# Optimization experiments

Measured on AMD Instinct MI355X. Metric: run time of the kernel, lower is better.

Reference implementation:

```python
import jax, jax.numpy as jnp
import numpy as np

OUT_FEATURES = 4096
IN_FEATURES = 4096
BLOCK_DIM = 16
K = 64
N_BLOCKS = OUT_FEATURES * IN_FEATURES // BLOCK_DIM  # 1,048,576


def setup_inputs() -> dict:
    key = jax.random.key(0)
    k1, k2, k3, k4, k5, k6 = jax.random.split(key, 6)
    x = jax.random.normal(k1, (8192, IN_FEATURES), dtype=jnp.float32)
    coarse_centroids = jax.random.normal(k2, (K, BLOCK_DIM), dtype=jnp.float32)
    coarse_labels = jax.random.randint(k3, (N_BLOCKS,), 0, K, dtype=jnp.int64)
    res_centroids = jax.random.normal(k4, (K, BLOCK_DIM), dtype=jnp.float32) * 0.1
    res_labels = jax.random.randint(k5, (N_BLOCKS,), 0, K, dtype=jnp.int64)
    bias = jax.random.normal(k6, (OUT_FEATURES,), dtype=jnp.float32)
    return {
        'x': x,
        'coarse_centroids': coarse_centroids,
        'coarse_labels': coarse_labels,
        'res_centroids': res_centroids,
        'res_labels': res_labels,
        'bias': bias,
    }


def _dequantize(coarse_centroids, coarse_labels, res_centroids, res_labels):
    # two-level VQ: coarse lookup + residual correction, per block of BLOCK_DIM
    blocks = coarse_centroids[coarse_labels] + res_centroids[res_labels]  # [N_BLOCKS, BLOCK_DIM]
    return blocks.reshape(OUT_FEATURES, IN_FEATURES)


def reference(x, coarse_centroids, coarse_labels, res_centroids, res_labels, bias):
    W = _dequantize(coarse_centroids, coarse_labels, res_centroids, res_labels)
    # F.linear: x @ W.T + bias
    return jnp.dot(x, W.T) + bias
```

## Files before the change

### kernel.cpp

```cpp
#include <hip/hip_runtime.h>
#include <hip/hip_bf16.h>
#include <stdint.h>

#define M_DIM 8192
#define N_DIM 4096
#define K_DIM 4096
#define BM 256
#define BN 256
#define BK2 64
#define NT2 (K_DIM / BK2)
#define THREADS 512
#define NBLOCKS_VQ (N_DIM * K_DIM / 16)

#define TILE_B 32768
#define BBASE  65536
#define SMEM_BYTES 131072

typedef short bf16x8 __attribute__((ext_vector_type(8)));
typedef float f32x4 __attribute__((ext_vector_type(4)));
typedef unsigned short ushort_t;
typedef ushort_t ushort8 __attribute__((ext_vector_type(8)));

#define GLOBAL_AS __attribute__((address_space(1)))
#define LDS_AS __attribute__((address_space(3)))

__device__ __forceinline__ ushort_t f2bf(float f) {
  union { float f; uint32_t u; } v; v.f = f;
  uint32_t u = v.u;
  return (ushort_t)((u + 0x7FFFu + ((u >> 16) & 1u)) >> 16);
}

__global__ __launch_bounds__(256) void dequant_w(
    const float* __restrict__ cc, const int* __restrict__ cl,
    const float* __restrict__ rc, const int* __restrict__ rl,
    ushort_t* __restrict__ wout) {
  int b = blockIdx.x * 256 + threadIdx.x;
  int ci = cl[b];
  int ri = rl[b];
  const float4* c4 = (const float4*)(cc + (size_t)ci * 16);
  const float4* r4 = (const float4*)(rc + (size_t)ri * 16);
  float s[16];
#pragma unroll
  for (int p = 0; p < 4; ++p) {
    float4 a = c4[p];
    float4 r = r4[p];
    s[p * 4 + 0] = a.x + r.x;
    s[p * 4 + 1] = a.y + r.y;
    s[p * 4 + 2] = a.z + r.z;
    s[p * 4 + 3] = a.w + r.w;
  }
  ushort8 o0, o1;
#pragma unroll
  for (int j = 0; j < 8; ++j) o0[j] = f2bf(s[j]);
#pragma unroll
  for (int j = 0; j < 8; ++j) o1[j] = f2bf(s[8 + j]);
  ushort8* dst = (ushort8*)(wout + (size_t)b * 16);
  dst[0] = o0;
  dst[1] = o1;
}

__global__ __launch_bounds__(256) void cvt_x_bf16(const float* __restrict__ x,
                                                  ushort_t* __restrict__ xb) {
  size_t i = (size_t)blockIdx.x * 256 + threadIdx.x;
  const float4* p = (const float4*)x + i * 2;
  float4 a = p[0];
  float4 b = p[1];
  ushort8 o;
  o[0] = f2bf(a.x); o[1] = f2bf(a.y); o[2] = f2bf(a.z); o[3] = f2bf(a.w);
  o[4] = f2bf(b.x); o[5] = f2bf(b.y); o[6] = f2bf(b.z); o[7] = f2bf(b.w);
  ((ushort8*)xb)[i] = o;
}

__device__ __forceinline__ void stage_tile(char* smem,
    const ushort_t* gA0, const ushort_t* gB0, int wbase, int tile, int buf) {
  const ushort_t* ga = gA0 + (size_t)tile * BK2;
  const ushort_t* gb = gB0 + (size_t)tile * BK2;
  char* la = smem + buf * TILE_B + wbase;
  char* lb = smem + BBASE + buf * TILE_B + wbase;
#pragma unroll
  for (int r = 0; r < 4; ++r) {
    __builtin_amdgcn_global_load_lds(
        (const GLOBAL_AS void*)(ga + (size_t)(r * 64) * K_DIM),
        (LDS_AS void*)(la + r * 8192), 16, 0, 0);
    __builtin_amdgcn_global_load_lds(
        (const GLOBAL_AS void*)(gb + (size_t)(r * 64) * K_DIM),
        (LDS_AS void*)(lb + r * 8192), 16, 0, 0);
  }
}

template<int VM, bool ISSUE>
__device__ __forceinline__ void kstep(char* smem,
    const ushort_t* gA0, const ushort_t* gB0, int wbase,
    int aBase, int bBase, f32x4 (&acc)[8][4], int t, int buf) {
  if constexpr (VM == 8) asm volatile("s_waitcnt vmcnt(8)" ::: "memory");
  else asm volatile("s_waitcnt vmcnt(0)" ::: "memory");
  __builtin_amdgcn_s_barrier();
  __builtin_amdgcn_sched_barrier(0);

  const ushort_t* aB = (const ushort_t*)(smem + buf * TILE_B) + aBase;
  const ushort_t* bB = (const ushort_t*)(smem + BBASE + buf * TILE_B) + bBase;

#pragma unroll
  for (int kk = 0; kk < 2; ++kk) {
    bf16x8 b[4], a[8];
#pragma unroll
    for (int n = 0; n < 4; ++n) b[n] = *(const bf16x8*)(bB + kk * 32 + n * 1024);
#pragma unroll
    for (int m = 0; m < 8; ++m) a[m] = *(const bf16x8*)(aB + kk * 32 + m * 1024);
    __builtin_amdgcn_s_setprio(1);
#pragma unroll
    for (int m = 0; m < 8; ++m)
#pragma unroll
      for (int n = 0; n < 4; ++n)
        acc[m][n] = __builtin_amdgcn_mfma_f32_16x16x32_bf16(a[m], b[n], acc[m][n], 0, 0, 0);
    __builtin_amdgcn_s_setprio(0);
  }
  __builtin_amdgcn_s_barrier();
  __builtin_amdgcn_sched_barrier(0);
  if constexpr (ISSUE)
    stage_tile(smem, gA0, gB0, wbase, t + 2, buf);
}

__global__ __launch_bounds__(THREADS, 2) void gemm_bf16(
    const ushort_t* __restrict__ A, const ushort_t* __restrict__ B,
    const float* __restrict__ bias, float* __restrict__ C) {
  extern __shared__ char smem[];

  const int nwg = (M_DIM / BM) * (N_DIM / BN);
  int bid = blockIdx.x;
  int swz = (bid & 7) * (nwg >> 3) + (bid >> 3);
  int bx = swz & 15;
  int by = swz >> 4;
  const int tileM = by * BM;
  const int tileN = bx * BN;

  const int tid = threadIdx.x;
  const int lane = tid & 63;
  const int wave = tid >> 6;
  const int wr = wave >> 2;
  const int wc = wave & 3;

  int srow = tid >> 3;
  int slot = tid & 7;
  int scol = ((slot ^ ((((unsigned)srow >> 2) & 1) << 1)) << 3);
  const ushort_t* gA0 = A + (size_t)(tileM + srow) * K_DIM + scol;
  const ushort_t* gB0 = B + (size_t)(tileN + srow) * K_DIM + scol;
  const int wbase = wave << 10;

  const int lrow = lane & 15;
  const int g8 = (lane >> 4) << 3;
  const int kx = g8 ^ ((lrow & 4) << 2);
  const int aBase = (wr * 128 + lrow) * 64 + kx;
  const int bBase = (wc * 64 + lrow) * 64 + kx;

  f32x4 acc[8][4];
#pragma unroll
  for (int m = 0; m < 8; ++m)
#pragma unroll
    for (int n = 0; n < 4; ++n) acc[m][n] = (f32x4)0.0f;

  stage_tile(smem, gA0, gB0, wbase, 0, 0);
  stage_tile(smem, gA0, gB0, wbase, 1, 1);

  for (int tb = 0; tb < 31; ++tb) {
    kstep<8, true>(smem, gA0, gB0, wbase, aBase, bBase, acc, 2 * tb, 0);
    kstep<8, true>(smem, gA0, gB0, wbase, aBase, bBase, acc, 2 * tb + 1, 1);
  }
  kstep<8, false>(smem, gA0, gB0, wbase, aBase, bBase, acc, 62, 0);
  kstep<0, false>(smem, gA0, gB0, wbase, aBase, bBase, acc, 63, 1);

  const int orow = tileM + wr * 128 + ((lane >> 4) << 2);
  const int ocol0 = tileN + wc * 64 + lrow;
  float bv[4];
#pragma unroll
  for (int n = 0; n < 4; ++n) bv[n] = bias[ocol0 + n * 16];
#pragma unroll
  for (int m = 0; m < 8; ++m) {
#pragma unroll
    for (int n = 0; n < 4; ++n) {
      size_t base = (size_t)(orow + m * 16) * N_DIM + (ocol0 + n * 16);
#pragma unroll
      for (int r = 0; r < 4; ++r)
        C[base + (size_t)r * N_DIM] = acc[m][n][r] + bv[n];
    }
  }
}

extern "C" void kernel_launch(void* const* d_in, const int* in_sizes, int n_in,
                              void* d_out, int out_size, void* d_ws, size_t ws_size,
                              hipStream_t stream) {
  const float* x = (const float*)d_in[0];
  const float* cc = (const float*)d_in[1];
  const int* cl = (const int*)d_in[2];
  const float* rc = (const float*)d_in[3];
  const int* rl = (const int*)d_in[4];
  const float* bias = (const float*)d_in[5];
  float* out = (float*)d_out;

  ushort_t* Wbf = (ushort_t*)d_ws;
  ushort_t* Xbf = (ushort_t*)d_ws + (size_t)N_DIM * K_DIM;

  (void)hipFuncSetAttribute((const void*)gemm_bf16,
                            hipFuncAttributeMaxDynamicSharedMemorySize, SMEM_BYTES);

  dequant_w<<<NBLOCKS_VQ / 256, 256, 0, stream>>>(cc, cl, rc, rl, Wbf);
  cvt_x_bf16<<<(int)((M_DIM * (size_t)K_DIM / 8) / 256), 256, 0, stream>>>(x, Xbf);
  gemm_bf16<<<(M_DIM / BM) * (N_DIM / BN), THREADS, SMEM_BYTES, stream>>>(Xbf, Wbf, bias, out);
}
```

Baseline: 299.4 us.

## Split GEMM k-tile into four quadrant phases interleaving loads with MFMAs

Replaces the two-stage k-step loop, which issued whole-tile prefetches after the compute, with a four-phase k-tile. Each phase reads part of the A/B fragments from LDS, issues part of the next tile's global-to-LDS loads, and runs a quarter of the MFMAs. The LDS swizzle also changes to a full XOR-by-row scheme, and the B rows are remapped so each phase reads one half of the tile. The aim is finer overlap of memory traffic with MFMA work and fewer LDS bank conflicts, at the cost of more barriers per k-tile and a single prefetch tile of lookahead instead of two.

```diff
diff --git a/kernel.cpp b/kernel.cpp
--- a/kernel.cpp
+++ b/kernel.cpp
@@ -7,13 +7,13 @@
 #define K_DIM 4096
 #define BM 256
 #define BN 256
-#define BK2 64
-#define NT2 (K_DIM / BK2)
+#define BK 64
+#define NT (K_DIM / BK)
 #define THREADS 512
 #define NBLOCKS_VQ (N_DIM * K_DIM / 16)
 
-#define TILE_B 32768
-#define BBASE  65536
+#define ABUF_B 32768
+#define BREG   65536
 #define SMEM_BYTES 131072
 
 typedef short bf16x8 __attribute__((ext_vector_type(8)));
@@ -71,54 +71,91 @@
   ((ushort8*)xb)[i] = o;
 }
 
-__device__ __forceinline__ void stage_tile(char* smem,
-    const ushort_t* gA0, const ushort_t* gB0, int wbase, int tile, int buf) {
-  const ushort_t* ga = gA0 + (size_t)tile * BK2;
-  const ushort_t* gb = gB0 + (size_t)tile * BK2;
-  char* la = smem + buf * TILE_B + wbase;
-  char* lb = smem + BBASE + buf * TILE_B + wbase;
-#pragma unroll
-  for (int r = 0; r < 4; ++r) {
-    __builtin_amdgcn_global_load_lds(
-        (const GLOBAL_AS void*)(ga + (size_t)(r * 64) * K_DIM),
-        (LDS_AS void*)(la + r * 8192), 16, 0, 0);
-    __builtin_amdgcn_global_load_lds(
-        (const GLOBAL_AS void*)(gb + (size_t)(r * 64) * K_DIM),
-        (LDS_AS void*)(lb + r * 8192), 16, 0, 0);
-  }
-}
-
-template<int VM, bool ISSUE>
-__device__ __forceinline__ void kstep(char* smem,
-    const ushort_t* gA0, const ushort_t* gB0, int wbase,
-    int aBase, int bBase, f32x4 (&acc)[8][4], int t, int buf) {
-  if constexpr (VM == 8) asm volatile("s_waitcnt vmcnt(8)" ::: "memory");
-  else asm volatile("s_waitcnt vmcnt(0)" ::: "memory");
-  __builtin_amdgcn_s_barrier();
-  __builtin_amdgcn_sched_barrier(0);
-
-  const ushort_t* aB = (const ushort_t*)(smem + buf * TILE_B) + aBase;
-  const ushort_t* bB = (const ushort_t*)(smem + BBASE + buf * TILE_B) + bBase;
-
-#pragma unroll
-  for (int kk = 0; kk < 2; ++kk) {
-    bf16x8 b[4], a[8];
-#pragma unroll
-    for (int n = 0; n < 4; ++n) b[n] = *(const bf16x8*)(bB + kk * 32 + n * 1024);
-#pragma unroll
-    for (int m = 0; m < 8; ++m) a[m] = *(const bf16x8*)(aB + kk * 32 + m * 1024);
-    __builtin_amdgcn_s_setprio(1);
-#pragma unroll
-    for (int m = 0; m < 8; ++m)
-#pragma unroll
-      for (int n = 0; n < 4; ++n)
-        acc[m][n] = __builtin_amdgcn_mfma_f32_16x16x32_bf16(a[m], b[n], acc[m][n], 0, 0, 0);
-    __builtin_amdgcn_s_setprio(0);
-  }
-  __builtin_amdgcn_s_barrier();
-  __builtin_amdgcn_sched_barrier(0);
-  if constexpr (ISSUE)
-    stage_tile(smem, gA0, gB0, wbase, t + 2, buf);
+struct SP {
+  const ushort_t* gA;
+  const ushort_t* gB;
+  char* sm;
+  int wuni;
+};
+
+__device__ __forceinline__ void stA(const SP& s, int r, int tile, int dbuf) {
+  __builtin_amdgcn_global_load_lds(
+      (const GLOBAL_AS void*)(s.gA + (size_t)tile * BK + (size_t)r * 64 * K_DIM),
+      (LDS_AS void*)(s.sm + dbuf * ABUF_B + r * 8192 + s.wuni), 16, 0, 0);
+}
+__device__ __forceinline__ void stB(const SP& s, int r, int tile, int dbuf) {
+  constexpr int roff[4] = {0, 128, 32, 160};
+  __builtin_amdgcn_global_load_lds(
+      (const GLOBAL_AS void*)(s.gB + (size_t)tile * BK + (size_t)roff[r] * K_DIM),
+      (LDS_AS void*)(s.sm + BREG + dbuf * ABUF_B + r * 8192 + s.wuni), 16, 0, 0);
+}
+
+#define BAR()  __builtin_amdgcn_s_barrier()
+#define SCB()  __builtin_amdgcn_sched_barrier(0)
+#define LGKM0() do { asm volatile("s_waitcnt lgkmcnt(0)" ::: "memory"); SCB(); } while (0)
+#define VMC(n) asm volatile("s_waitcnt vmcnt(" #n ")" ::: "memory")
+
+#define MFMA_Q(ACCM, AARR, BARR, ACCN)                                         \
+  __builtin_amdgcn_s_setprio(1);                                               \
+  _Pragma("unroll")                                                            \
+  for (int m = 0; m < 4; ++m)                                                  \
+    _Pragma("unroll")                                                          \
+    for (int ni = 0; ni < 2; ++ni) {                                           \
+      acc[ACCM + m][ACCN + ni] = __builtin_amdgcn_mfma_f32_16x16x32_bf16(      \
+          AARR[m * 2 + 0], BARR[ni * 2 + 0], acc[ACCM + m][ACCN + ni], 0, 0, 0); \
+      acc[ACCM + m][ACCN + ni] = __builtin_amdgcn_mfma_f32_16x16x32_bf16(      \
+          AARR[m * 2 + 1], BARR[ni * 2 + 1], acc[ACCM + m][ACCN + ni], 0, 0, 0); \
+    }                                                                          \
+  __builtin_amdgcn_s_setprio(0);
+
+template<bool ISSUE, int VMP2, int VMP4>
+__device__ __forceinline__ void ktile(const SP& sp, int buf, int t,
+    int aBase, int bBase, int sw0, int sw1, f32x4 (&acc)[8][4]) {
+  const ushort_t* bufA = (const ushort_t*)(sp.sm + buf * ABUF_B);
+  const ushort_t* bufB = (const ushort_t*)(sp.sm + BREG + buf * ABUF_B);
+  bf16x8 a[8], b0[4], b1[4];
+
+#pragma unroll
+  for (int m = 0; m < 4; ++m) {
+    a[m * 2 + 0] = *(const bf16x8*)(bufA + aBase + m * 1024 + sw0);
+    a[m * 2 + 1] = *(const bf16x8*)(bufA + aBase + m * 1024 + sw1);
+  }
+#pragma unroll
+  for (int ni = 0; ni < 2; ++ni) {
+    b0[ni * 2 + 0] = *(const bf16x8*)(bufB + bBase + ni * 1024 + sw0);
+    b0[ni * 2 + 1] = *(const bf16x8*)(bufB + bBase + ni * 1024 + sw1);
+  }
+  if constexpr (ISSUE) { stB(sp, 0, t + 1, buf ^ 1); stB(sp, 1, t + 1, buf ^ 1); }
+  BAR(); LGKM0();
+  MFMA_Q(0, a, b0, 0);
+  BAR(); SCB();
+
+#pragma unroll
+  for (int ni = 0; ni < 2; ++ni) {
+    b1[ni * 2 + 0] = *(const bf16x8*)(bufB + bBase + 8192 + ni * 1024 + sw0);
+    b1[ni * 2 + 1] = *(const bf16x8*)(bufB + bBase + 8192 + ni * 1024 + sw1);
+  }
+  if constexpr (ISSUE) { stB(sp, 2, t + 1, buf ^ 1); stB(sp, 3, t + 1, buf ^ 1); }
+  if constexpr (VMP2 == 4) VMC(4); else VMC(0);
+  BAR(); LGKM0();
+  MFMA_Q(0, a, b1, 2);
+  BAR(); SCB();
+
+#pragma unroll
+  for (int m = 0; m < 4; ++m) {
+    a[m * 2 + 0] = *(const bf16x8*)(bufA + aBase + 4096 + m * 1024 + sw0);
+    a[m * 2 + 1] = *(const bf16x8*)(bufA + aBase + 4096 + m * 1024 + sw1);
+  }
+  if constexpr (ISSUE) { stA(sp, 0, t + 1, buf ^ 1); stA(sp, 2, t + 1, buf ^ 1); }
+  BAR(); LGKM0();
+  MFMA_Q(4, a, b0, 0);
+  BAR(); SCB();
+
+  if constexpr (ISSUE) { stA(sp, 1, t + 1, buf ^ 1); stA(sp, 3, t + 1, buf ^ 1); }
+  if constexpr (VMP4 == 2) VMC(2); else VMC(0);
+  BAR(); LGKM0();
+  MFMA_Q(4, a, b1, 2);
+  BAR(); SCB();
 }
 
 __global__ __launch_bounds__(THREADS, 2) void gemm_bf16(
@@ -137,21 +174,26 @@
   const int tid = threadIdx.x;
   const int lane = tid & 63;
   const int wave = tid >> 6;
-  const int wr = wave >> 2;
-  const int wc = wave & 3;
-
-  int srow = tid >> 3;
+  const int wrM = wave >> 2;
+  const int wcN = wave & 3;
+
+  int q = tid >> 3;
   int slot = tid & 7;
-  int scol = ((slot ^ ((((unsigned)srow >> 2) & 1) << 1)) << 3);
-  const ushort_t* gA0 = A + (size_t)(tileM + srow) * K_DIM + scol;
-  const ushort_t* gB0 = B + (size_t)(tileN + srow) * K_DIM + scol;
-  const int wbase = wave << 10;
+  int scol = ((slot ^ (q & 7)) << 3);
+  SP sp;
+  sp.sm = smem;
+  sp.wuni = wave << 10;
+  sp.gA = A + (size_t)(tileM + q) * K_DIM + scol;
+  int rB0 = ((q >> 5) << 6) + (q & 31);
+  sp.gB = B + (size_t)(tileN + rB0) * K_DIM + scol;
 
   const int lrow = lane & 15;
-  const int g8 = (lane >> 4) << 3;
-  const int kx = g8 ^ ((lrow & 4) << 2);
-  const int aBase = (wr * 128 + lrow) * 64 + kx;
-  const int bBase = (wc * 64 + lrow) * 64 + kx;
+  const int g = lane >> 4;
+  const int l7 = lane & 7;
+  const int sw0 = ((g ^ l7) << 3);
+  const int sw1 = (((4 + g) ^ l7) << 3);
+  const int aBase = (wrM * 128 + lrow) * 64;
+  const int bBase = (wcN * 32 + lrow) * 64;
 
   f32x4 acc[8][4];
 #pragma unroll
@@ -159,18 +201,17 @@
 #pragma unroll
     for (int n = 0; n < 4; ++n) acc[m][n] = (f32x4)0.0f;
 
-  stage_tile(smem, gA0, gB0, wbase, 0, 0);
-  stage_tile(smem, gA0, gB0, wbase, 1, 1);
-
-  for (int tb = 0; tb < 31; ++tb) {
-    kstep<8, true>(smem, gA0, gB0, wbase, aBase, bBase, acc, 2 * tb, 0);
-    kstep<8, true>(smem, gA0, gB0, wbase, aBase, bBase, acc, 2 * tb + 1, 1);
-  }
-  kstep<8, false>(smem, gA0, gB0, wbase, aBase, bBase, acc, 62, 0);
-  kstep<0, false>(smem, gA0, gB0, wbase, aBase, bBase, acc, 63, 1);
-
-  const int orow = tileM + wr * 128 + ((lane >> 4) << 2);
-  const int ocol0 = tileN + wc * 64 + lrow;
+  stB(sp, 0, 0, 0); stB(sp, 1, 0, 0); stB(sp, 2, 0, 0); stB(sp, 3, 0, 0);
+  stA(sp, 0, 0, 0); stA(sp, 2, 0, 0); stA(sp, 1, 0, 0); stA(sp, 3, 0, 0);
+  VMC(2);
+  BAR(); SCB();
+
+  for (int t = 0; t < NT - 1; ++t)
+    ktile<true, 4, 2>(sp, t & 1, t, aBase, bBase, sw0, sw1, acc);
+  ktile<false, 0, 0>(sp, (NT - 1) & 1, NT - 1, aBase, bBase, sw0, sw1, acc);
+
+  const int orow = tileM + wrM * 128 + ((lane >> 4) << 2);
+  const int ocol0 = tileN + wcN * 64 + lrow;
   float bv[4];
 #pragma unroll
   for (int n = 0; n < 4; ++n) bv[n] = bias[ocol0 + n * 16];
```

New measurement: 292.7 us. 1.02x faster.
